# Optimization experiments

Hardware: AMD Instinct MI355X
Metric: run time of the kernel (lower is better)

## Reference

```python
import jax, jax.numpy as jnp
import numpy as np

N, B, S, E, D, L, H, OUT = 16384, 32, 512, 262144, 256, 4, 4, 768
DH = D // H
ATOM_VOCABS = [119, 9, 12, 12, 10, 6, 9, 2, 2]
BOND_VOCABS = [22, 6, 2]
BN_EPS = 1e-5


def bn(x, g, b):
    # BatchNorm1d over nodes (training-mode statistics, deterministic)
    mu = x.mean(0)
    var = ((x - mu) ** 2).mean(0)
    return (x - mu) * jax.lax.rsqrt(var + BN_EPS) * g + b


def setup_inputs():
    key = jax.random.key(0)
    ks = iter(jax.random.split(key, 80))
    x = jnp.stack([jax.random.randint(next(ks), (N,), 0, v) for v in ATOM_VOCABS], 1)
    edge_attr = jnp.stack([jax.random.randint(next(ks), (E,), 0, v) for v in BOND_VOCABS], 1)
    epg = E // B  # edges per graph, edges stay within their graph
    gid = jnp.arange(E) // epg
    src = jax.random.randint(next(ks), (E,), 0, S) + gid * S
    dst = jax.random.randint(next(ks), (E,), 0, S) + gid * S
    edge_index = jnp.stack([src, dst], 0)
    batch_vec = jnp.arange(N) // S  # B equal-sized graphs, contiguous

    def rn(shape, std=0.02):
        return jax.random.normal(next(ks), shape, jnp.float32) * std

    inp = dict(x=x, edge_attr=edge_attr, edge_index=edge_index, batch_vec=batch_vec)
    inp['atom_tab'] = rn((len(ATOM_VOCABS), max(ATOM_VOCABS), D))
    inp['bond_tab'] = rn((len(BOND_VOCABS), max(BOND_VOCABS), D))
    inp['elin_w'] = rn((L, D, D)); inp['elin_b'] = jnp.zeros((L, D))
    inp['eps'] = jnp.zeros((L,))  # GINE train_eps init 0
    inp['gw1'] = rn((L, D, 2 * D)); inp['gb1'] = jnp.zeros((L, 2 * D))
    inp['gw2'] = rn((L, 2 * D, D)); inp['gb2'] = jnp.zeros((L, D))
    inp['aw_in'] = rn((L, D, 3 * D)); inp['ab_in'] = jnp.zeros((L, 3 * D))
    inp['aw_out'] = rn((L, D, D)); inp['ab_out'] = jnp.zeros((L, D))
    for n in ('n1', 'n2', 'n3'):
        inp[n + 'g'] = jnp.ones((L, D)); inp[n + 'b'] = jnp.zeros((L, D))
    inp['mw1'] = rn((L, D, 2 * D)); inp['mb1'] = jnp.zeros((L, 2 * D))
    inp['mw2'] = rn((L, 2 * D, D)); inp['mb2'] = jnp.zeros((L, D))
    inp['pw1'] = rn((D, D)); inp['pb1'] = jnp.zeros((D,))
    inp['pw2'] = rn((D, OUT)); inp['pb2'] = jnp.zeros((OUT,))
    return inp


def forward(x, edge_attr, edge_index, batch_vec, atom_tab, bond_tab, elin_w, elin_b, eps,
            gw1, gb1, gw2, gb2, aw_in, ab_in, aw_out, ab_out,
            n1g, n1b, n2g, n2b, n3g, n3b, mw1, mb1, mw2, mb2,
            pw1, pb1, pw2, pb2):
    # AtomEncoder / BondEncoder: sum of per-feature embeddings
    h = atom_tab[jnp.arange(atom_tab.shape[0])[None, :], x].sum(1)      # [N, D]
    e = bond_tab[jnp.arange(bond_tab.shape[0])[None, :], edge_attr].sum(1)  # [E, D]
    src, dst = edge_index[0], edge_index[1]
    scale = 1.0 / np.sqrt(DH)
    for l in range(L):
        # --- GINEConv local branch ---
        el = e @ elin_w[l] + elin_b[l]                       # edge lin
        msg = jax.nn.relu(h[src] + el)                       # [E, D]
        agg = jax.ops.segment_sum(msg, dst, num_segments=N)  # scatter-add
        hc = (1.0 + eps[l]) * h + agg
        hc = jax.nn.relu(hc @ gw1[l] + gb1[l]) @ gw2[l] + gb2[l]
        hc = bn(hc + h, n1g[l], n1b[l])
        # --- global multihead attention (dense per-graph batch, all slots valid) ---
        hd = h.reshape(B, S, D)
        qkv = hd @ aw_in[l] + ab_in[l]
        q, k, v = jnp.split(qkv, 3, axis=-1)
        q = q.reshape(B, S, H, DH).transpose(0, 2, 1, 3)
        k = k.reshape(B, S, H, DH).transpose(0, 2, 1, 3)
        v = v.reshape(B, S, H, DH).transpose(0, 2, 1, 3)
        attn = jax.nn.softmax(jnp.einsum('bhqd,bhkd->bhqk', q, k) * scale, axis=-1)
        ao = jnp.einsum('bhqk,bhkd->bhqd', attn, v).transpose(0, 2, 1, 3).reshape(N, D)
        ao = ao @ aw_out[l] + ab_out[l]
        ha = bn(ao + h, n2g[l], n2b[l])
        # --- combine + MLP ---
        out = hc + ha
        out = out + (jax.nn.relu(out @ mw1[l] + mb1[l]) @ mw2[l] + mb2[l])
        h = bn(out, n3g[l], n3b[l])
    # global mean pool
    counts = jax.ops.segment_sum(jnp.ones((N, 1), h.dtype), batch_vec, num_segments=B)
    g = jax.ops.segment_sum(h, batch_vec, num_segments=B) / counts
    z = jax.nn.relu(g @ pw1 + pb1) @ pw2 + pb2
    return z / jnp.linalg.norm(z, axis=-1, keepdims=True)


def reference(x, edge_attr, edge_index, batch_vec, atom_tab, bond_tab, elin_w, elin_b, eps,
              gw1, gb1, gw2, gb2, aw_in, ab_in, aw_out, ab_out,
              n1g, n1b, n2g, n2b, n3g, n3b, mw1, mb1, mw2, mb2,
              pw1, pb1, pw2, pb2):
    return forward(x, edge_attr, edge_index, batch_vec, atom_tab, bond_tab, elin_w, elin_b, eps,
                   gw1, gb1, gw2, gb2, aw_in, ab_in, aw_out, ab_out,
                   n1g, n1b, n2g, n2b, n3g, n3b, mw1, mb1, mw2, mb2,
                   pw1, pb1, pw2, pb2)
```

## Files before the change

### kernel.cpp

```cpp
#include <hip/hip_runtime.h>
#include <hip/hip_bf16.h>
#include <math.h>

#define N_NODES 16384
#define NB      32
#define S_PG    512
#define NE      262144
#define EPG     8192
#define D       256
#define D2      512
#define D3      768
#define NL      4
#define NH      4
#define DHD     64
#define OUTD    768
#define NCOMBO  264
#define WT_PER_LAYER 786432
#define INV_N   (1.0f / (float)N_NODES)
#define QSCALE  0.1803368801111244f

typedef short s8v __attribute__((ext_vector_type(8)));
typedef float f4v __attribute__((ext_vector_type(4)));

__device__ __forceinline__ unsigned bfr(float f) {
    unsigned u = __float_as_uint(f);
    return (u + 0x7fffu + ((u >> 16) & 1u)) >> 16;
}
__device__ __forceinline__ float b2f(unsigned short u) {
    return __uint_as_float(((unsigned)u) << 16);
}

__global__ __launch_bounds__(256) void k_atom_enc(const int* __restrict__ x,
                                                  const float* __restrict__ tab,
                                                  float* __restrict__ h,
                                                  unsigned short* __restrict__ hb) {
    int node = blockIdx.x * 4 + (threadIdx.x >> 6);
    int lane = threadIdx.x & 63;
    int dd = lane << 2;
    float4 acc = {0.f, 0.f, 0.f, 0.f};
#pragma unroll
    for (int f = 0; f < 9; ++f) {
        int v = x[node * 9 + f];
        const float4 t = *(const float4*)&tab[((size_t)(f * 119 + v)) * D + dd];
        acc.x += t.x; acc.y += t.y; acc.z += t.z; acc.w += t.w;
    }
    *(float4*)&h[(size_t)node * D + dd] = acc;
    ushort4 o;
    o.x = (unsigned short)bfr(acc.x); o.y = (unsigned short)bfr(acc.y);
    o.z = (unsigned short)bfr(acc.z); o.w = (unsigned short)bfr(acc.w);
    *(ushort4*)&hb[(size_t)node * D + dd] = o;
}

__global__ __launch_bounds__(256) void k_bondw(const float* __restrict__ bond_tab,
                                               const float* __restrict__ elin_w,
                                               float* __restrict__ bw) {
    int blk = blockIdx.x;
    int l = blk / 66, fv = blk % 66;
    int dout = threadIdx.x;
    const float* tabrow = bond_tab + (size_t)fv * D;
    const float* w = elin_w + (size_t)l * D * D;
    float acc = 0.f;
    for (int d = 0; d < D; ++d) acc = fmaf(tabrow[d], w[d * D + dout], acc);
    bw[((size_t)l * 66 + fv) * D + dout] = acc;
}

__global__ __launch_bounds__(256) void k_combo(const float* __restrict__ bw,
                                               const float* __restrict__ elin_b,
                                               unsigned short* __restrict__ ctb) {
    int b = blockIdx.x;
    int l = b / NCOMBO, cid = b % NCOMBO;
    int a0 = cid / 12, a1 = (cid % 12) / 2, a2 = cid & 1;
    int d = threadIdx.x;
    const float* bwl = bw + (size_t)l * 66 * D;
    float v = bwl[(size_t)a0 * D + d] + bwl[(size_t)(22 + a1) * D + d] +
              bwl[(size_t)(44 + a2) * D + d] + elin_b[(size_t)l * D + d];
    ctb[((size_t)l * NCOMBO + cid) * D + d] = (unsigned short)bfr(v);
}

__global__ __launch_bounds__(256) void k_zero16k(int* __restrict__ p) {
    p[blockIdx.x * 256 + threadIdx.x] = 0;
}
__global__ __launch_bounds__(256) void k_zero_stats12(float* __restrict__ p) {
    for (int i = 0; i < 24; ++i) p[i * 256 + threadIdx.x] = 0.f;
}
__global__ __launch_bounds__(256) void k_hist(const int* __restrict__ dst, int* __restrict__ deg) {
    int e = blockIdx.x * 256 + threadIdx.x;
    atomicAdd(&deg[dst[e]], 1);
}
__global__ __launch_bounds__(256) void k_scan(const int* __restrict__ deg,
                                              int* __restrict__ row_ptr,
                                              int* __restrict__ cursor) {
    __shared__ int partial[256];
    int t = threadIdx.x;
    int base = t * 64;
    int s = 0;
    for (int i = 0; i < 64; ++i) s += deg[base + i];
    partial[t] = s;
    __syncthreads();
    for (int dstp = 1; dstp < 256; dstp <<= 1) {
        int v = (t >= dstp) ? partial[t - dstp] : 0;
        __syncthreads();
        partial[t] += v;
        __syncthreads();
    }
    int run = partial[t] - s;
    for (int i = 0; i < 64; ++i) {
        int dcur = deg[base + i];
        row_ptr[base + i] = run;
        cursor[base + i] = run;
        run += dcur;
    }
    if (t == 255) row_ptr[N_NODES] = run;
}
__global__ __launch_bounds__(256) void k_scatter(const int* __restrict__ src,
                                                 const int* __restrict__ dst,
                                                 const int* __restrict__ ea,
                                                 int* __restrict__ cursor,
                                                 int2* __restrict__ sorted) {
    int e = blockIdx.x * 256 + threadIdx.x;
    int d = dst[e];
    int pos = atomicAdd(&cursor[d], 1);
    int cid = ea[e * 3] * 12 + ea[e * 3 + 1] * 2 + ea[e * 3 + 2];
    sorted[pos] = make_int2(src[e], cid);
}

__global__ __launch_bounds__(256) void k_gine_agg(const unsigned short* __restrict__ hb,
                                                  const float* __restrict__ h,
                                                  const unsigned short* __restrict__ ctb,
                                                  const float* __restrict__ eps, int l,
                                                  const int* __restrict__ row_ptr,
                                                  const int2* __restrict__ sorted,
                                                  unsigned short* __restrict__ aggb) {
    int w = threadIdx.x >> 6;
    int lane = threadIdx.x & 63;
    int n = blockIdx.x * 4 + w;
    int dd = lane << 2;
    int beg = row_ptr[n], end = row_ptr[n + 1];
    float4 acc = {0.f, 0.f, 0.f, 0.f};
    int i = beg;
    for (; i + 2 <= end; i += 2) {
        int2 e0 = sorted[i];
        int2 e1 = sorted[i + 1];
        ushort4 h0 = *(const ushort4*)&hb[(size_t)e0.x * D + dd];
        ushort4 c0 = *(const ushort4*)&ctb[(size_t)e0.y * D + dd];
        ushort4 h1 = *(const ushort4*)&hb[(size_t)e1.x * D + dd];
        ushort4 c1 = *(const ushort4*)&ctb[(size_t)e1.y * D + dd];
        acc.x += fmaxf(b2f(h0.x) + b2f(c0.x), 0.f) + fmaxf(b2f(h1.x) + b2f(c1.x), 0.f);
        acc.y += fmaxf(b2f(h0.y) + b2f(c0.y), 0.f) + fmaxf(b2f(h1.y) + b2f(c1.y), 0.f);
        acc.z += fmaxf(b2f(h0.z) + b2f(c0.z), 0.f) + fmaxf(b2f(h1.z) + b2f(c1.z), 0.f);
        acc.w += fmaxf(b2f(h0.w) + b2f(c0.w), 0.f) + fmaxf(b2f(h1.w) + b2f(c1.w), 0.f);
    }
    if (i < end) {
        int2 e0 = sorted[i];
        ushort4 h0 = *(const ushort4*)&hb[(size_t)e0.x * D + dd];
        ushort4 c0 = *(const ushort4*)&ctb[(size_t)e0.y * D + dd];
        acc.x += fmaxf(b2f(h0.x) + b2f(c0.x), 0.f);
        acc.y += fmaxf(b2f(h0.y) + b2f(c0.y), 0.f);
        acc.z += fmaxf(b2f(h0.z) + b2f(c0.z), 0.f);
        acc.w += fmaxf(b2f(h0.w) + b2f(c0.w), 0.f);
    }
    float s1p = 1.f + eps[l];
    float4 hn = *(const float4*)&h[(size_t)n * D + dd];
    ushort4 o;
    o.x = (unsigned short)bfr(s1p * hn.x + acc.x);
    o.y = (unsigned short)bfr(s1p * hn.y + acc.y);
    o.z = (unsigned short)bfr(s1p * hn.z + acc.z);
    o.w = (unsigned short)bfr(s1p * hn.w + acc.w);
    *(ushort4*)&aggb[(size_t)n * D + dd] = o;
}

__global__ __launch_bounds__(256) void k_wcvt(const float* __restrict__ gw1, const float* __restrict__ gw2,
                                              const float* __restrict__ aw_in, const float* __restrict__ aw_out,
                                              const float* __restrict__ mw1, const float* __restrict__ mw2,
                                              unsigned short* __restrict__ WT) {
    const int KS[6]   = {256, 512, 256, 256, 256, 512};
    const int NS[6]   = {512, 256, 768, 256, 512, 256};
    const int TOFF[7] = {0, 128, 256, 448, 512, 640, 768};
    const int DOFF[6] = {0, 131072, 262144, 458752, 524288, 655360};
    int b = blockIdx.x;
    int l = b / 768, wb = b % 768;
    int widx = 0;
    while (wb >= TOFF[widx + 1]) ++widx;
    int t = wb - TOFF[widx];
    int K = KS[widx], N = NS[widx];
    int nn = N / 32;
    int kt = t / nn, nt = t % nn;
    const float* srcs[6] = {gw1, gw2, aw_in, aw_out, mw1, mw2};
    const float* W = srcs[widx] + (size_t)l * K * N;
    unsigned short* WTp = WT + (size_t)l * WT_PER_LAYER + DOFF[widx];
    __shared__ float tile[32][33];
    int tid = threadIdx.x;
    int r = tid >> 3, c4 = (tid & 7) << 2;
    float4 v = *(const float4*)&W[(size_t)(kt * 32 + r) * N + nt * 32 + c4];
    tile[r][c4] = v.x; tile[r][c4 + 1] = v.y; tile[r][c4 + 2] = v.z; tile[r][c4 + 3] = v.w;
    __syncthreads();
    int nr = tid >> 3, kc = (tid & 7) << 2;
    ushort4 o;
    o.x = (unsigned short)bfr(tile[kc + 0][nr]);
    o.y = (unsigned short)bfr(tile[kc + 1][nr]);
    o.z = (unsigned short)bfr(tile[kc + 2][nr]);
    o.w = (unsigned short)bfr(tile[kc + 3][nr]);
    *(ushort4*)&WTp[(size_t)(nt * 32 + nr) * K + kt * 32 + kc] = o;
}

template<int RELU, int RES, int OBF, int STAT>
__global__ __launch_bounds__(256) void k_mm2(const unsigned short* __restrict__ A,
                                             const unsigned short* __restrict__ BT,
                                             const float* __restrict__ bias,
                                             const float* __restrict__ res,
                                             void* __restrict__ Cp,
                                             float* __restrict__ stat,
                                             int M, int N, int K) {
    __shared__ unsigned short As[128 * 64];
    __shared__ unsigned short Bs[128 * 64];
    const int tid = threadIdx.x;
    const int row0 = blockIdx.y * 128, col0 = blockIdx.x * 128;
    const int w = tid >> 6, l = tid & 63;
    const int wm = w >> 1, wn = w & 1;
    const int lr = l & 15, lq = l >> 4;
    const int srow = l >> 3;
    const int scol = (l & 7) * 8;
    f4v acc[4][4] = {};

    const unsigned short* Ag = A + (size_t)(row0 + w * 32 + srow) * K + scol;
    const unsigned short* Bg = BT + (size_t)(col0 + w * 32 + srow) * K + scol;
    unsigned short* Al = &As[(w * 32) * 64];
    unsigned short* Bl = &Bs[(w * 32) * 64];

    for (int k0 = 0; k0 < K; k0 += 64) {
#pragma unroll
        for (int it = 0; it < 4; ++it) {
            __builtin_amdgcn_global_load_lds(
                (const __attribute__((address_space(1))) unsigned*)(Ag + (size_t)(it * 8) * K + k0),
                (__attribute__((address_space(3))) unsigned*)(Al + it * 8 * 64), 16, 0, 0);
            __builtin_amdgcn_global_load_lds(
                (const __attribute__((address_space(1))) unsigned*)(Bg + (size_t)(it * 8) * K + k0),
                (__attribute__((address_space(3))) unsigned*)(Bl + it * 8 * 64), 16, 0, 0);
        }
        asm volatile("s_waitcnt vmcnt(0)" ::: "memory");
        __syncthreads();
#pragma unroll
        for (int kk = 0; kk < 2; ++kk) {
            s8v af[4], bf[4];
#pragma unroll
            for (int m = 0; m < 4; ++m)
                af[m] = *(const s8v*)&As[(wm * 64 + m * 16 + lr) * 64 + kk * 32 + lq * 8];
#pragma unroll
            for (int n = 0; n < 4; ++n)
                bf[n] = *(const s8v*)&Bs[(wn * 64 + n * 16 + lr) * 64 + kk * 32 + lq * 8];
#pragma unroll
            for (int m = 0; m < 4; ++m)
#pragma unroll
                for (int n = 0; n < 4; ++n)
                    acc[m][n] = __builtin_amdgcn_mfma_f32_16x16x32_bf16(af[m], bf[n], acc[m][n], 0, 0, 0);
        }
        __syncthreads();
    }
    float cs[4], cs2[4];
#pragma unroll
    for (int n = 0; n < 4; ++n) { cs[n] = 0.f; cs2[n] = 0.f; }
#pragma unroll
    for (int n = 0; n < 4; ++n) {
        int c = col0 + wn * 64 + n * 16 + lr;
        float bv = bias[c];
#pragma unroll
        for (int m = 0; m < 4; ++m) {
#pragma unroll
            for (int j = 0; j < 4; ++j) {
                int r = row0 + wm * 64 + m * 16 + lq * 4 + j;
                float v = acc[m][n][j] + bv;
                if (RES) v += res[(size_t)r * N + c];
                if (STAT) { cs[n] += v; cs2[n] += v * v; }
                if (RELU) v = fmaxf(v, 0.f);
                if (OBF) ((unsigned short*)Cp)[(size_t)r * N + c] = (unsigned short)bfr(v);
                else ((float*)Cp)[(size_t)r * N + c] = v;
            }
        }
    }
    if (STAT) {
#pragma unroll
        for (int n = 0; n < 4; ++n) {
            float s = cs[n], s2 = cs2[n];
            s += __shfl_xor(s, 16);  s2 += __shfl_xor(s2, 16);
            s += __shfl_xor(s, 32);  s2 += __shfl_xor(s2, 32);
            if (lq == 0) {
                int c = col0 + wn * 64 + n * 16 + lr;
                atomicAdd(&stat[c], s);
                atomicAdd(&stat[256 + c], s2);
            }
        }
    }
}

__global__ __launch_bounds__(256) void k_mm2_dual(const unsigned short* __restrict__ A1,
                                                  const unsigned short* __restrict__ B1,
                                                  const float* __restrict__ bias1,
                                                  unsigned short* __restrict__ C1, int N1, int nb1,
                                                  const unsigned short* __restrict__ A2,
                                                  const unsigned short* __restrict__ B2,
                                                  const float* __restrict__ bias2,
                                                  unsigned short* __restrict__ C2, int N2,
                                                  int K) {
    __shared__ unsigned short As[128 * 64];
    __shared__ unsigned short Bs[128 * 64];
    const unsigned short* A; const unsigned short* BT; const float* bias;
    unsigned short* C; int N, cb, relu;
    if ((int)blockIdx.x < nb1) { A = A1; BT = B1; bias = bias1; C = C1; N = N1; cb = blockIdx.x; relu = 1; }
    else { A = A2; BT = B2; bias = bias2; C = C2; N = N2; cb = blockIdx.x - nb1; relu = 0; }
    const int tid = threadIdx.x;
    const int row0 = blockIdx.y * 128, col0 = cb * 128;
    const int w = tid >> 6, l = tid & 63;
    const int wm = w >> 1, wn = w & 1;
    const int lr = l & 15, lq = l >> 4;
    const int srow = l >> 3;
    const int scol = (l & 7) * 8;
    f4v acc[4][4] = {};

    const unsigned short* Ag = A + (size_t)(row0 + w * 32 + srow) * K + scol;
    const unsigned short* Bg = BT + (size_t)(col0 + w * 32 + srow) * K + scol;
    unsigned short* Al = &As[(w * 32) * 64];
    unsigned short* Bl = &Bs[(w * 32) * 64];

    for (int k0 = 0; k0 < K; k0 += 64) {
#pragma unroll
        for (int it = 0; it < 4; ++it) {
            __builtin_amdgcn_global_load_lds(
                (const __attribute__((address_space(1))) unsigned*)(Ag + (size_t)(it * 8) * K + k0),
                (__attribute__((address_space(3))) unsigned*)(Al + it * 8 * 64), 16, 0, 0);
            __builtin_amdgcn_global_load_lds(
                (const __attribute__((address_space(1))) unsigned*)(Bg + (size_t)(it * 8) * K + k0),
                (__attribute__((address_space(3))) unsigned*)(Bl + it * 8 * 64), 16, 0, 0);
        }
        asm volatile("s_waitcnt vmcnt(0)" ::: "memory");
        __syncthreads();
#pragma unroll
        for (int kk = 0; kk < 2; ++kk) {
            s8v af[4], bf[4];
#pragma unroll
            for (int m = 0; m < 4; ++m)
                af[m] = *(const s8v*)&As[(wm * 64 + m * 16 + lr) * 64 + kk * 32 + lq * 8];
#pragma unroll
            for (int n = 0; n < 4; ++n)
                bf[n] = *(const s8v*)&Bs[(wn * 64 + n * 16 + lr) * 64 + kk * 32 + lq * 8];
#pragma unroll
            for (int m = 0; m < 4; ++m)
#pragma unroll
                for (int n = 0; n < 4; ++n)
                    acc[m][n] = __builtin_amdgcn_mfma_f32_16x16x32_bf16(af[m], bf[n], acc[m][n], 0, 0, 0);
        }
        __syncthreads();
    }
#pragma unroll
    for (int n = 0; n < 4; ++n) {
        int c = col0 + wn * 64 + n * 16 + lr;
        float bv = bias[c];
#pragma unroll
        for (int m = 0; m < 4; ++m) {
#pragma unroll
            for (int j = 0; j < 4; ++j) {
                int r = row0 + wm * 64 + m * 16 + lq * 4 + j;
                float v = acc[m][n][j] + bv;
                if (relu) v = fmaxf(v, 0.f);
                else if (c < 256) v *= QSCALE;
                C[(size_t)r * N + c] = (unsigned short)bfr(v);
            }
        }
    }
}

template<int RELU, int RES, int OBF, int STAT>
__global__ __launch_bounds__(256) void k_mm64(const unsigned short* __restrict__ A,
                                              const unsigned short* __restrict__ BT,
                                              const float* __restrict__ bias,
                                              const float* __restrict__ res,
                                              void* __restrict__ Cp,
                                              float* __restrict__ stat,
                                              int M, int N, int K) {
    __shared__ unsigned short As[64 * 64];
    __shared__ unsigned short Bs[128 * 64];
    const int tid = threadIdx.x;
    const int row0 = blockIdx.y * 64, col0 = blockIdx.x * 128;
    const int w = tid >> 6, l = tid & 63;
    const int wn = w;
    const int lr = l & 15, lq = l >> 4;
    const int srow = l >> 3;
    const int scol = (l & 7) * 8;
    f4v acc[4][2] = {};

    const unsigned short* Ag = A + (size_t)(row0 + w * 16 + srow) * K + scol;
    const unsigned short* Bg = BT + (size_t)(col0 + w * 32 + srow) * K + scol;
    unsigned short* Al = &As[(w * 16) * 64];
    unsigned short* Bl = &Bs[(w * 32) * 64];

    for (int k0 = 0; k0 < K; k0 += 64) {
#pragma unroll
        for (int it = 0; it < 2; ++it)
            __builtin_amdgcn_global_load_lds(
                (const __attribute__((address_space(1))) unsigned*)(Ag + (size_t)(it * 8) * K + k0),
                (__attribute__((address_space(3))) unsigned*)(Al + it * 8 * 64), 16, 0, 0);
#pragma unroll
        for (int it = 0; it < 4; ++it)
            __builtin_amdgcn_global_load_lds(
                (const __attribute__((address_space(1))) unsigned*)(Bg + (size_t)(it * 8) * K + k0),
                (__attribute__((address_space(3))) unsigned*)(Bl + it * 8 * 64), 16, 0, 0);
        asm volatile("s_waitcnt vmcnt(0)" ::: "memory");
        __syncthreads();
#pragma unroll
        for (int kk = 0; kk < 2; ++kk) {
            s8v af[4], bf[2];
#pragma unroll
            for (int m = 0; m < 4; ++m)
                af[m] = *(const s8v*)&As[(m * 16 + lr) * 64 + kk * 32 + lq * 8];
#pragma unroll
            for (int n = 0; n < 2; ++n)
                bf[n] = *(const s8v*)&Bs[(wn * 32 + n * 16 + lr) * 64 + kk * 32 + lq * 8];
#pragma unroll
            for (int m = 0; m < 4; ++m)
#pragma unroll
                for (int n = 0; n < 2; ++n)
                    acc[m][n] = __builtin_amdgcn_mfma_f32_16x16x32_bf16(af[m], bf[n], acc[m][n], 0, 0, 0);
        }
        __syncthreads();
    }
    float cs[2], cs2[2];
#pragma unroll
    for (int n = 0; n < 2; ++n) { cs[n] = 0.f; cs2[n] = 0.f; }
#pragma unroll
    for (int n = 0; n < 2; ++n) {
        int c = col0 + wn * 32 + n * 16 + lr;
        float bv = bias[c];
#pragma unroll
        for (int m = 0; m < 4; ++m) {
#pragma unroll
            for (int j = 0; j < 4; ++j) {
                int r = row0 + m * 16 + lq * 4 + j;
                float v = acc[m][n][j] + bv;
                if (RES) v += res[(size_t)r * N + c];
                if (STAT) { cs[n] += v; cs2[n] += v * v; }
                if (RELU) v = fmaxf(v, 0.f);
                if (OBF) ((unsigned short*)Cp)[(size_t)r * N + c] = (unsigned short)bfr(v);
                else ((float*)Cp)[(size_t)r * N + c] = v;
            }
        }
    }
    if (STAT) {
#pragma unroll
        for (int n = 0; n < 2; ++n) {
            float s = cs[n], s2 = cs2[n];
            s += __shfl_xor(s, 16);  s2 += __shfl_xor(s2, 16);
            s += __shfl_xor(s, 32);  s2 += __shfl_xor(s2, 32);
            if (lq == 0) {
                int c = col0 + wn * 32 + n * 16 + lr;
                atomicAdd(&stat[c], s);
                atomicAdd(&stat[256 + c], s2);
            }
        }
    }
}

__global__ __launch_bounds__(256) void k_mm64_dual(const unsigned short* __restrict__ A1,
                                                   const unsigned short* __restrict__ B1,
                                                   const float* __restrict__ bias1,
                                                   const float* __restrict__ res1,
                                                   float* __restrict__ C1,
                                                   float* __restrict__ stat1, int K1, int nb1,
                                                   const unsigned short* __restrict__ A2,
                                                   const unsigned short* __restrict__ B2,
                                                   const float* __restrict__ bias2,
                                                   const float* __restrict__ res2,
                                                   float* __restrict__ C2,
                                                   float* __restrict__ stat2, int K2) {
    __shared__ unsigned short As[64 * 64];
    __shared__ unsigned short Bs[128 * 64];
    const unsigned short *A, *BT; const float *bias, *res; float *C, *stat;
    int K, cb;
    if ((int)blockIdx.x < nb1) { A = A1; BT = B1; bias = bias1; res = res1; C = C1; stat = stat1; K = K1; cb = blockIdx.x; }
    else { A = A2; BT = B2; bias = bias2; res = res2; C = C2; stat = stat2; K = K2; cb = blockIdx.x - nb1; }
    const int N = 256;
    const int tid = threadIdx.x;
    const int row0 = blockIdx.y * 64, col0 = cb * 128;
    const int w = tid >> 6, l = tid & 63;
    const int wn = w;
    const int lr = l & 15, lq = l >> 4;
    const int srow = l >> 3;
    const int scol = (l & 7) * 8;
    f4v acc[4][2] = {};

    const unsigned short* Ag = A + (size_t)(row0 + w * 16 + srow) * K + scol;
    const unsigned short* Bg = BT + (size_t)(col0 + w * 32 + srow) * K + scol;
    unsigned short* Al = &As[(w * 16) * 64];
    unsigned short* Bl = &Bs[(w * 32) * 64];

    for (int k0 = 0; k0 < K; k0 += 64) {
#pragma unroll
        for (int it = 0; it < 2; ++it)
            __builtin_amdgcn_global_load_lds(
                (const __attribute__((address_space(1))) unsigned*)(Ag + (size_t)(it * 8) * K + k0),
                (__attribute__((address_space(3))) unsigned*)(Al + it * 8 * 64), 16, 0, 0);
#pragma unroll
        for (int it = 0; it < 4; ++it)
            __builtin_amdgcn_global_load_lds(
                (const __attribute__((address_space(1))) unsigned*)(Bg + (size_t)(it * 8) * K + k0),
                (__attribute__((address_space(3))) unsigned*)(Bl + it * 8 * 64), 16, 0, 0);
        asm volatile("s_waitcnt vmcnt(0)" ::: "memory");
        __syncthreads();
#pragma unroll
        for (int kk = 0; kk < 2; ++kk) {
            s8v af[4], bf[2];
#pragma unroll
            for (int m = 0; m < 4; ++m)
                af[m] = *(const s8v*)&As[(m * 16 + lr) * 64 + kk * 32 + lq * 8];
#pragma unroll
            for (int n = 0; n < 2; ++n)
                bf[n] = *(const s8v*)&Bs[(wn * 32 + n * 16 + lr) * 64 + kk * 32 + lq * 8];
#pragma unroll
            for (int m = 0; m < 4; ++m)
#pragma unroll
                for (int n = 0; n < 2; ++n)
                    acc[m][n] = __builtin_amdgcn_mfma_f32_16x16x32_bf16(af[m], bf[n], acc[m][n], 0, 0, 0);
        }
        __syncthreads();
    }
    float cs[2], cs2[2];
#pragma unroll
    for (int n = 0; n < 2; ++n) { cs[n] = 0.f; cs2[n] = 0.f; }
#pragma unroll
    for (int n = 0; n < 2; ++n) {
        int c = col0 + wn * 32 + n * 16 + lr;
        float bv = bias[c];
#pragma unroll
        for (int m = 0; m < 4; ++m) {
#pragma unroll
            for (int j = 0; j < 4; ++j) {
                int r = row0 + m * 16 + lq * 4 + j;
                float v = acc[m][n][j] + bv + res[(size_t)r * N + c];
                cs[n] += v; cs2[n] += v * v;
                C[(size_t)r * N + c] = v;
            }
        }
    }
#pragma unroll
    for (int n = 0; n < 2; ++n) {
        float s = cs[n], s2 = cs2[n];
        s += __shfl_xor(s, 16);  s2 += __shfl_xor(s2, 16);
        s += __shfl_xor(s, 32);  s2 += __shfl_xor(s2, 32);
        if (lq == 0) {
            int c = col0 + wn * 32 + n * 16 + lr;
            atomicAdd(&stat[c], s);
            atomicAdd(&stat[256 + c], s2);
        }
    }
}

__global__ __launch_bounds__(256) void k_bn12i(const float* __restrict__ t1,
                                               const float* __restrict__ sa1,
                                               const float* __restrict__ g1,
                                               const float* __restrict__ b1,
                                               const float* __restrict__ t2,
                                               const float* __restrict__ sa2,
                                               const float* __restrict__ g2,
                                               const float* __restrict__ b2,
                                               float* __restrict__ y,
                                               unsigned short* __restrict__ yb) {
    size_t i4 = (size_t)blockIdx.x * blockDim.x + threadIdx.x;
    int c = (int)((i4 & 63) << 2);
    float a1[4], a2[4], o[4];
    *(float4*)a1 = ((const float4*)t1)[i4];
    *(float4*)a2 = ((const float4*)t2)[i4];
#pragma unroll
    for (int q = 0; q < 4; ++q) {
        int cc = c + q;
        float m1 = sa1[cc] * INV_N;
        float r1 = rsqrtf(sa1[256 + cc] * INV_N - m1 * m1 + 1e-5f);
        float m2 = sa2[cc] * INV_N;
        float r2 = rsqrtf(sa2[256 + cc] * INV_N - m2 * m2 + 1e-5f);
        o[q] = (a1[q] - m1) * r1 * g1[cc] + b1[cc] + (a2[q] - m2) * r2 * g2[cc] + b2[cc];
    }
    ((float4*)y)[i4] = *(float4*)o;
    ushort4 ob;
    ob.x = (unsigned short)bfr(o[0]); ob.y = (unsigned short)bfr(o[1]);
    ob.z = (unsigned short)bfr(o[2]); ob.w = (unsigned short)bfr(o[3]);
    ((ushort4*)yb)[i4] = ob;
}

__global__ __launch_bounds__(256) void k_bn_apply_i(const float* __restrict__ x,
                                                    const float* __restrict__ sa,
                                                    const float* __restrict__ g,
                                                    const float* __restrict__ b,
                                                    float* __restrict__ y,
                                                    unsigned short* __restrict__ yb) {
    size_t i4 = (size_t)blockIdx.x * blockDim.x + threadIdx.x;
    int c = (int)((i4 & 63) << 2);
    float a[4], o[4];
    *(float4*)a = ((const float4*)x)[i4];
#pragma unroll
    for (int q = 0; q < 4; ++q) {
        int cc = c + q;
        float m = sa[cc] * INV_N;
        float r = rsqrtf(sa[256 + cc] * INV_N - m * m + 1e-5f);
        o[q] = (a[q] - m) * r * g[cc] + b[cc];
    }
    ((float4*)y)[i4] = *(float4*)o;
    ushort4 ob;
    ob.x = (unsigned short)bfr(o[0]); ob.y = (unsigned short)bfr(o[1]);
    ob.z = (unsigned short)bfr(o[2]); ob.w = (unsigned short)bfr(o[3]);
    ((ushort4*)yb)[i4] = ob;
}

__global__ __launch_bounds__(256) void k_flash_mfma(const unsigned short* __restrict__ qkv,
                                                    unsigned short* __restrict__ ao) {
    __shared__ unsigned short Ks[64][72];
    __shared__ unsigned short VT[64][72];
    __shared__ unsigned short Ps[4][2][16][72];
    const int bh = blockIdx.x;
    const int b = bh >> 2, hh = bh & 3;
    const int i0 = blockIdx.y << 7;
    const int tid = threadIdx.x;
    const int w = tid >> 6, l = tid & 63;
    const int lr = l & 15, lq = l >> 4;
    const int hd = hh * DHD;
    const size_t rowbase = (size_t)(b * S_PG) * D3;

    s8v aq[2][2];
#pragma unroll
    for (int g = 0; g < 2; ++g) {
        const unsigned short* qrow = &qkv[rowbase + (size_t)(i0 + g * 64 + w * 16 + lr) * D3 + hd + lq * 8];
        aq[g][0] = *(const s8v*)&qrow[0];
        aq[g][1] = *(const s8v*)&qrow[32];
    }

    float mrow[2][4], lrow[2][4];
    f4v oacc[2][4] = {};
#pragma unroll
    for (int g = 0; g < 2; ++g)
#pragma unroll
        for (int j = 0; j < 4; ++j) { mrow[g][j] = -INFINITY; lrow[g][j] = 0.f; }

    const int skv = tid >> 2;
    const int sd0 = (tid & 3) << 4;
    const int d0v = (tid >> 4) << 2;
    const int kv0 = (tid & 15) << 2;

    for (int j0 = 0; j0 < S_PG; j0 += 64) {
        __syncthreads();
        {
            const unsigned short* kr = &qkv[rowbase + (size_t)(j0 + skv) * D3 + D + hd + sd0];
            *(uint4*)&Ks[skv][sd0]     = *(const uint4*)&kr[0];
            *(uint4*)&Ks[skv][sd0 + 8] = *(const uint4*)&kr[8];
            unsigned short vv[4][4];
#pragma unroll
            for (int i = 0; i < 4; ++i) {
                uint2 lv = *(const uint2*)&qkv[rowbase + (size_t)(j0 + kv0 + i) * D3 + D2 + hd + d0v];
                vv[i][0] = (unsigned short)(lv.x & 0xffffu);
                vv[i][1] = (unsigned short)(lv.x >> 16);
                vv[i][2] = (unsigned short)(lv.y & 0xffffu);
                vv[i][3] = (unsigned short)(lv.y >> 16);
            }
#pragma unroll
            for (int i2 = 0; i2 < 4; ++i2) {
                ushort4 o4;
                o4.x = vv[0][i2]; o4.y = vv[1][i2]; o4.z = vv[2][i2]; o4.w = vv[3][i2];
                *(ushort4*)&VT[d0v + i2][kv0] = o4;
            }
        }
        __syncthreads();
#pragma unroll
        for (int g = 0; g < 2; ++g) {
            f4v sc[4] = {};
#pragma unroll
            for (int nt = 0; nt < 4; ++nt) {
                s8v bk0 = *(const s8v*)&Ks[nt * 16 + lr][lq * 8];
                s8v bk1 = *(const s8v*)&Ks[nt * 16 + lr][32 + lq * 8];
                sc[nt] = __builtin_amdgcn_mfma_f32_16x16x32_bf16(aq[g][0], bk0, sc[nt], 0, 0, 0);
                sc[nt] = __builtin_amdgcn_mfma_f32_16x16x32_bf16(aq[g][1], bk1, sc[nt], 0, 0, 0);
            }
            float ps[4][4], alpha[4];
#pragma unroll
            for (int j = 0; j < 4; ++j) {
#pragma unroll
                for (int nt = 0; nt < 4; ++nt) ps[nt][j] = sc[nt][j];
                float pm = fmaxf(fmaxf(ps[0][j], ps[1][j]), fmaxf(ps[2][j], ps[3][j]));
#pragma unroll
                for (int off = 1; off < 16; off <<= 1) pm = fmaxf(pm, __shfl_xor(pm, off));
                float mn = fmaxf(mrow[g][j], pm);
                alpha[j] = exp2f(mrow[g][j] - mn);
                float rs = 0.f;
#pragma unroll
                for (int nt = 0; nt < 4; ++nt) { ps[nt][j] = exp2f(ps[nt][j] - mn); rs += ps[nt][j]; }
#pragma unroll
                for (int off = 1; off < 16; off <<= 1) rs += __shfl_xor(rs, off);
                lrow[g][j] = lrow[g][j] * alpha[j] + rs;
                mrow[g][j] = mn;
            }
#pragma unroll
            for (int nt = 0; nt < 4; ++nt)
#pragma unroll
                for (int j = 0; j < 4; ++j)
                    Ps[w][g][lq * 4 + j][nt * 16 + lr] = (unsigned short)bfr(ps[nt][j]);
#pragma unroll
            for (int ntd = 0; ntd < 4; ++ntd)
#pragma unroll
                for (int j = 0; j < 4; ++j) oacc[g][ntd][j] *= alpha[j];
            s8v pa0 = *(const s8v*)&Ps[w][g][lr][lq * 8];
            s8v pa1 = *(const s8v*)&Ps[w][g][lr][32 + lq * 8];
#pragma unroll
            for (int ntd = 0; ntd < 4; ++ntd) {
                s8v bv0 = *(const s8v*)&VT[ntd * 16 + lr][lq * 8];
                s8v bv1 = *(const s8v*)&VT[ntd * 16 + lr][32 + lq * 8];
                oacc[g][ntd] = __builtin_amdgcn_mfma_f32_16x16x32_bf16(pa0, bv0, oacc[g][ntd], 0, 0, 0);
                oacc[g][ntd] = __builtin_amdgcn_mfma_f32_16x16x32_bf16(pa1, bv1, oacc[g][ntd], 0, 0, 0);
            }
        }
    }
#pragma unroll
    for (int g = 0; g < 2; ++g)
#pragma unroll
        for (int j = 0; j < 4; ++j) {
            float inv = 1.f / lrow[g][j];
            int node = b * S_PG + i0 + g * 64 + w * 16 + lq * 4 + j;
#pragma unroll
            for (int ntd = 0; ntd < 4; ++ntd)
                ao[(size_t)node * D + hd + ntd * 16 + lr] = (unsigned short)bfr(oacc[g][ntd][j] * inv);
        }
}

__global__ __launch_bounds__(256) void k_pool2(const float* __restrict__ h, float* __restrict__ g) {
    __shared__ float red[8][33];
    int b = blockIdx.x, cc = blockIdx.y;
    int col = threadIdx.x & 31, rg = threadIdx.x >> 5;
    const float* p = h + ((size_t)(b * S_PG + rg * 64)) * D + cc * 32 + col;
    float s = 0.f;
    for (int r = 0; r < 64; ++r) s += p[(size_t)r * D];
    red[rg][col] = s;
    __syncthreads();
    if (rg == 0) {
        float t = 0.f;
#pragma unroll
        for (int i = 0; i < 8; ++i) t += red[i][col];
        g[b * D + cc * 32 + col] = t * (1.f / (float)S_PG);
    }
}

__global__ __launch_bounds__(256) void k_final_a(const float* __restrict__ g,
                                                 const float* __restrict__ pw1,
                                                 const float* __restrict__ pb1,
                                                 const float* __restrict__ pw2,
                                                 const float* __restrict__ pb2,
                                                 float* __restrict__ z,
                                                 float* __restrict__ zpart) {
    __shared__ float gs[D];
    __shared__ float ts[D];
    __shared__ float red[4];
    int b = blockIdx.x, ch = blockIdx.y, tid = threadIdx.x;
    gs[tid] = g[b * D + tid];
    __syncthreads();
    float acc = pb1[tid];
    for (int d = 0; d < D; ++d) acc = fmaf(gs[d], pw1[d * D + tid], acc);
    ts[tid] = fmaxf(acc, 0.f);
    __syncthreads();
    int j = ch * 256 + tid;
    float a = pb2[j];
    for (int d = 0; d < D; ++d) a = fmaf(ts[d], pw2[(size_t)d * OUTD + j], a);
    z[b * OUTD + j] = a;
    float ss = a * a;
#pragma unroll
    for (int o = 32; o >= 1; o >>= 1) ss += __shfl_xor(ss, o);
    if ((tid & 63) == 0) red[tid >> 6] = ss;
    __syncthreads();
    if (tid == 0) zpart[b * 3 + ch] = red[0] + red[1] + red[2] + red[3];
}

__global__ __launch_bounds__(256) void k_final_b(const float* __restrict__ z,
                                                 const float* __restrict__ zpart,
                                                 float* __restrict__ out) {
    int b = blockIdx.x, ch = blockIdx.y, tid = threadIdx.x;
    float rn = rsqrtf(zpart[b * 3] + zpart[b * 3 + 1] + zpart[b * 3 + 2]);
    int j = ch * 256 + tid;
    out[b * OUTD + j] = z[b * OUTD + j] * rn;
}

extern "C" void kernel_launch(void* const* d_in, const int* in_sizes, int n_in,
                              void* d_out, int out_size, void* d_ws, size_t ws_size,
                              hipStream_t stream) {
    const int* x        = (const int*)d_in[0];
    const int* ea       = (const int*)d_in[1];
    const int* eidx     = (const int*)d_in[2];
    const float* atom_tab = (const float*)d_in[4];
    const float* bond_tab = (const float*)d_in[5];
    const float* elin_w = (const float*)d_in[6];
    const float* elin_b = (const float*)d_in[7];
    const float* eps    = (const float*)d_in[8];
    const float* gw1    = (const float*)d_in[9];
    const float* gb1    = (const float*)d_in[10];
    const float* gw2    = (const float*)d_in[11];
    const float* gb2    = (const float*)d_in[12];
    const float* aw_in  = (const float*)d_in[13];
    const float* ab_in  = (const float*)d_in[14];
    const float* aw_out = (const float*)d_in[15];
    const float* ab_out = (const float*)d_in[16];
    const float* n1g    = (const float*)d_in[17];
    const float* n1b    = (const float*)d_in[18];
    const float* n2g    = (const float*)d_in[19];
    const float* n2b    = (const float*)d_in[20];
    const float* n3g    = (const float*)d_in[21];
    const float* n3b    = (const float*)d_in[22];
    const float* mw1    = (const float*)d_in[23];
    const float* mb1    = (const float*)d_in[24];
    const float* mw2    = (const float*)d_in[25];
    const float* mb2    = (const float*)d_in[26];
    const float* pw1    = (const float*)d_in[27];
    const float* pb1    = (const float*)d_in[28];
    const float* pw2    = (const float*)d_in[29];
    const float* pb2    = (const float*)d_in[30];

    char* ws = (char*)d_ws;
    size_t off = 0;
    auto alloc = [&](size_t bytes) {
        void* p = ws + off;
        off += (bytes + 255) & ~(size_t)255;
        return p;
    };
    float*  h    = (float*)alloc((size_t)N_NODES * D * 4);
    float*  bufB = (float*)alloc((size_t)N_NODES * D * 4);
    float*  tmp1 = (float*)alloc((size_t)N_NODES * D * 4);
    unsigned short* hb = (unsigned short*)alloc((size_t)N_NODES * D * 2);
    char*   U    = (char*)alloc((size_t)N_NODES * D3 * 2);
    unsigned short* bfA = (unsigned short*)alloc((size_t)N_NODES * D3 * 2);
    unsigned short* WT  = (unsigned short*)alloc((size_t)NL * WT_PER_LAYER * 2);
    float*  bw   = (float*)alloc((size_t)NL * 66 * D * 4);
    unsigned short* ctb = (unsigned short*)alloc((size_t)NL * NCOMBO * D * 2);
    int*    deg  = (int*)alloc((size_t)N_NODES * 4);
    int*    row_ptr = (int*)alloc((size_t)(N_NODES + 1) * 4);
    int*    cursor  = (int*)alloc((size_t)N_NODES * 4);
    int2*   sorted  = (int2*)alloc((size_t)NE * 8);
    float*  statacc = (float*)alloc((size_t)12 * 512 * 4);
    float*  g    = (float*)alloc((size_t)NB * D * 4);
    float*  z    = (float*)alloc((size_t)NB * OUTD * 4);
    float*  zpart = (float*)alloc((size_t)NB * 3 * 4);
    (void)ws_size; (void)in_sizes; (void)n_in; (void)out_size;

    float* tmp23 = (float*)U;
    unsigned short* qkv = (unsigned short*)U;
    unsigned short* aggb  = bfA;
    unsigned short* ao    = bfA;
    unsigned short* bufBb = bfA;
    unsigned short* hid   = bfA + (size_t)N_NODES * D;

    const int* srcp = eidx;
    const int* dstp = eidx + NE;
    const int EW = N_NODES * D / 1024;

    k_zero16k<<<N_NODES / 256, 256, 0, stream>>>(deg);
    k_zero_stats12<<<1, 256, 0, stream>>>(statacc);
    k_hist<<<NE / 256, 256, 0, stream>>>(dstp, deg);
    k_scan<<<1, 256, 0, stream>>>(deg, row_ptr, cursor);
    k_scatter<<<NE / 256, 256, 0, stream>>>(srcp, dstp, ea, cursor, sorted);
    k_atom_enc<<<N_NODES / 4, 256, 0, stream>>>(x, atom_tab, h, hb);
    k_bondw<<<NL * 66, 256, 0, stream>>>(bond_tab, elin_w, bw);
    k_combo<<<NL * NCOMBO, 256, 0, stream>>>(bw, elin_b, ctb);
    k_wcvt<<<NL * 768, 256, 0, stream>>>(gw1, gw2, aw_in, aw_out, mw1, mw2, WT);

    for (int l = 0; l < NL; ++l) {
        const unsigned short* WTl = WT + (size_t)l * WT_PER_LAYER;
        float* sl0 = statacc + (size_t)(l * 3 + 0) * 512;
        float* sl1 = statacc + (size_t)(l * 3 + 1) * 512;
        float* sl2 = statacc + (size_t)(l * 3 + 2) * 512;
        k_gine_agg<<<N_NODES / 4, 256, 0, stream>>>(hb, h, ctb + (size_t)l * NCOMBO * D, eps, l,
                                                    row_ptr, sorted, aggb);
        k_mm2_dual<<<dim3(10, N_NODES / 128), 256, 0, stream>>>(
            aggb, WTl + 0, gb1 + (size_t)l * D2, hid, D2, 4,
            hb, WTl + 262144, ab_in + (size_t)l * D3, qkv, D3, D);
        k_flash_mfma<<<dim3(NB * NH, S_PG / 128), 256, 0, stream>>>(qkv, ao);
        k_mm64_dual<<<dim3(4, N_NODES / 64), 256, 0, stream>>>(
            hid, WTl + 131072, gb2 + (size_t)l * D, h, tmp1, sl0, D2, 2,
            ao, WTl + 458752, ab_out + (size_t)l * D, h, tmp23, sl1, D);
        k_bn12i<<<EW, 256, 0, stream>>>(tmp1, sl0, n1g + l * D, n1b + l * D,
                                        tmp23, sl1, n2g + l * D, n2b + l * D, bufB, bufBb);
        k_mm2<1, 0, 1, 0><<<dim3(D2 / 128, N_NODES / 128), 256, 0, stream>>>(
            bufBb, WTl + 524288, mb1 + (size_t)l * D2, nullptr, hid, nullptr, N_NODES, D2, D);
        k_mm64<0, 1, 0, 1><<<dim3(D / 128, N_NODES / 64), 256, 0, stream>>>(
            hid, WTl + 655360, mb2 + (size_t)l * D, bufB, tmp23, sl2, N_NODES, D, D2);
        k_bn_apply_i<<<EW, 256, 0, stream>>>(tmp23, sl2, n3g + l * D, n3b + l * D, h, hb);
    }
    k_pool2<<<dim3(NB, 8), 256, 0, stream>>>(h, g);
    k_final_a<<<dim3(NB, 3), 256, 0, stream>>>(g, pw1, pb1, pw2, pb2, z, zpart);
    k_final_b<<<dim3(NB, 3), 256, 0, stream>>>(z, zpart, (float*)d_out);
}
```

Before: 904.3 us.

## Split flash attention over KV halves with separate combine kernel

```diff
diff --git a/kernel.cpp b/kernel.cpp
--- a/kernel.cpp
+++ b/kernel.cpp
@@ -608,13 +608,15 @@
 }
 
 __global__ __launch_bounds__(256) void k_flash_mfma(const unsigned short* __restrict__ qkv,
-                                                    unsigned short* __restrict__ ao) {
+                                                    float* __restrict__ opart,
+                                                    float* __restrict__ ml) {
     __shared__ unsigned short Ks[64][72];
     __shared__ unsigned short VT[64][72];
     __shared__ unsigned short Ps[4][2][16][72];
     const int bh = blockIdx.x;
     const int b = bh >> 2, hh = bh & 3;
     const int i0 = blockIdx.y << 7;
+    const int z = blockIdx.z;
     const int tid = threadIdx.x;
     const int w = tid >> 6, l = tid & 63;
     const int lr = l & 15, lq = l >> 4;
@@ -641,7 +643,8 @@
     const int d0v = (tid >> 4) << 2;
     const int kv0 = (tid & 15) << 2;
 
-    for (int j0 = 0; j0 < S_PG; j0 += 64) {
+    const int jbeg = z * (S_PG / 2), jend = jbeg + S_PG / 2;
+    for (int j0 = jbeg; j0 < jend; j0 += 64) {
         __syncthreads();
         {
             const unsigned short* kr = &qkv[rowbase + (size_t)(j0 + skv) * D3 + D + hd + sd0];
@@ -712,16 +715,49 @@
             }
         }
     }
+    float* op = opart + (size_t)z * N_NODES * D;
 #pragma unroll
     for (int g = 0; g < 2; ++g)
 #pragma unroll
         for (int j = 0; j < 4; ++j) {
-            float inv = 1.f / lrow[g][j];
-            int node = b * S_PG + i0 + g * 64 + w * 16 + lq * 4 + j;
+            int rrow = i0 + g * 64 + w * 16 + lq * 4 + j;
+            int node = b * S_PG + rrow;
 #pragma unroll
             for (int ntd = 0; ntd < 4; ++ntd)
-                ao[(size_t)node * D + hd + ntd * 16 + lr] = (unsigned short)bfr(oacc[g][ntd][j] * inv);
-        }
+                op[(size_t)node * D + hd + ntd * 16 + lr] = oacc[g][ntd][j];
+            if (lr == 0) {
+                size_t mlidx = (((size_t)z * 128 + bh) * S_PG + rrow) * 2;
+                ml[mlidx] = mrow[g][j];
+                ml[mlidx + 1] = lrow[g][j];
+            }
+        }
+}
+
+__global__ __launch_bounds__(256) void k_flash_comb(const float* __restrict__ opart,
+                                                    const float* __restrict__ ml,
+                                                    unsigned short* __restrict__ ao) {
+    size_t i4 = (size_t)blockIdx.x * 256 + threadIdx.x;
+    int node = (int)(i4 >> 6);
+    int dpos = (int)(i4 & 63) << 2;
+    int head = dpos >> 6;
+    int b = node >> 9, rrow = node & 511;
+    int bh = (b << 2) | head;
+    size_t m1i = (((size_t)0 * 128 + bh) * S_PG + rrow) * 2;
+    size_t m2i = (((size_t)1 * 128 + bh) * S_PG + rrow) * 2;
+    float m1 = ml[m1i], l1 = ml[m1i + 1];
+    float m2 = ml[m2i], l2 = ml[m2i + 1];
+    float mm = fmaxf(m1, m2);
+    float w1 = exp2f(m1 - mm), w2 = exp2f(m2 - mm);
+    float inv = 1.f / (l1 * w1 + l2 * w2);
+    float s1 = w1 * inv, s2 = w2 * inv;
+    float4 o1 = *(const float4*)&opart[(size_t)node * D + dpos];
+    float4 o2 = *(const float4*)&opart[(size_t)N_NODES * D + (size_t)node * D + dpos];
+    ushort4 o;
+    o.x = (unsigned short)bfr(o1.x * s1 + o2.x * s2);
+    o.y = (unsigned short)bfr(o1.y * s1 + o2.y * s2);
+    o.z = (unsigned short)bfr(o1.z * s1 + o2.z * s2);
+    o.w = (unsigned short)bfr(o1.w * s1 + o2.w * s2);
+    *(ushort4*)&ao[(size_t)node * D + dpos] = o;
 }
 
 __global__ __launch_bounds__(256) void k_pool2(const float* __restrict__ h, float* __restrict__ g) {
@@ -834,6 +870,8 @@
     int*    cursor  = (int*)alloc((size_t)N_NODES * 4);
     int2*   sorted  = (int2*)alloc((size_t)NE * 8);
     float*  statacc = (float*)alloc((size_t)12 * 512 * 4);
+    float*  opart = (float*)alloc((size_t)2 * N_NODES * D * 4);
+    float*  ml    = (float*)alloc((size_t)2 * 128 * S_PG * 2 * 4);
     float*  g    = (float*)alloc((size_t)NB * D * 4);
     float*  z    = (float*)alloc((size_t)NB * OUTD * 4);
     float*  zpart = (float*)alloc((size_t)NB * 3 * 4);
@@ -870,7 +908,8 @@
         k_mm2_dual<<<dim3(10, N_NODES / 128), 256, 0, stream>>>(
             aggb, WTl + 0, gb1 + (size_t)l * D2, hid, D2, 4,
             hb, WTl + 262144, ab_in + (size_t)l * D3, qkv, D3, D);
-        k_flash_mfma<<<dim3(NB * NH, S_PG / 128), 256, 0, stream>>>(qkv, ao);
+        k_flash_mfma<<<dim3(NB * NH, S_PG / 128, 2), 256, 0, stream>>>(qkv, opart, ml);
+        k_flash_comb<<<N_NODES * D / 1024, 256, 0, stream>>>(opart, ml, ao);
         k_mm64_dual<<<dim3(4, N_NODES / 64), 256, 0, stream>>>(
             hid, WTl + 131072, gb2 + (size_t)l * D, h, tmp1, sl0, D2, 2,
             ao, WTl + 458752, ab_out + (size_t)l * D, h, tmp23, sl1, D);
```

After: 944.6 us. 1.04x slower.
